# Optimization experiments

Measured on AMD Instinct MI355X. Metric: run time of the kernel, lower is better.

The kernel has to match this reference:

```python
import jax, jax.numpy as jnp
import numpy as np
from jax import lax

EPS = 1e-5  # BatchNorm eps (eval mode, running stats)
HEADS = 8

# --- surrogate-gradient Heaviside (sigmoid surrogate, alpha=4) ---
@jax.custom_vjp
def spike(u):
    return (u >= 0.0).astype(u.dtype)

def _spike_fwd(u):
    return spike(u), u

def _spike_bwd(u, g):
    s = jax.nn.sigmoid(4.0 * u)
    return (g * 4.0 * s * (1.0 - s),)

spike.defvjp(_spike_fwd, _spike_bwd)

def lif(x, tau=0.5, threshold=1.0):
    """Multi-step LIF over leading time axis: v_t = tau*v_{t-1} + x_t,
    s_t = H(v_t - threshold), hard reset v_t *= (1 - s_t)."""
    def step(v, xt):
        v = tau * v + xt
        s = spike(v - threshold)
        return v * (1.0 - s), s
    _, out = lax.scan(step, jnp.zeros_like(x[0]), x)
    return out

def bn_eval(x, gamma, beta, mean, var):
    # x: (T,B,C,N); per-channel affine using running stats
    inv = gamma / jnp.sqrt(var + EPS)
    return x * inv[None, None, :, None] + (beta - mean * inv)[None, None, :, None]

def setup_inputs() -> dict:
    key = jax.random.key(0)
    ks = jax.random.split(key, 12)
    T, B, C, H, W = 4, 32, 384, 16, 16
    d = {}
    d['x'] = jax.random.normal(ks[0], (T, B, C, H, W), dtype=jnp.float32)
    # 1x1 Conv1d weights == (C_out, C_in) matrices
    sc = 1.0 / np.sqrt(C)
    d['q_w'] = jax.random.normal(ks[1], (C, C), dtype=jnp.float32) * sc
    d['q_gamma'] = jnp.ones((C,), jnp.float32)
    d['q_beta'] = jnp.zeros((C,), jnp.float32)
    d['q_mean'] = jax.random.normal(ks[2], (C,), dtype=jnp.float32) * 0.1
    d['q_var'] = jax.random.uniform(ks[3], (C,), dtype=jnp.float32) + 0.5
    d['k_w'] = jax.random.normal(ks[4], (C, C), dtype=jnp.float32) * sc
    d['k_gamma'] = jnp.ones((C,), jnp.float32)
    d['k_beta'] = jnp.zeros((C,), jnp.float32)
    d['k_mean'] = jax.random.normal(ks[5], (C,), dtype=jnp.float32) * 0.1
    d['k_var'] = jax.random.uniform(ks[6], (C,), dtype=jnp.float32) + 0.5
    d['proj_w'] = jax.random.normal(ks[7], (C, C), dtype=jnp.float32) * sc
    d['proj_b'] = jax.random.normal(ks[8], (C,), dtype=jnp.float32) * 0.01
    d['proj_gamma'] = jnp.ones((C,), jnp.float32)
    d['proj_beta'] = jnp.zeros((C,), jnp.float32)
    d['proj_mean'] = jax.random.normal(ks[9], (C,), dtype=jnp.float32) * 0.1
    d['proj_var'] = jax.random.uniform(ks[10], (C,), dtype=jnp.float32) + 0.5
    d['mem_alpha'] = jnp.float32(0.2)
    return d

def reference(x, q_w, q_gamma, q_beta, q_mean, q_var,
              k_w, k_gamma, k_beta, k_mean, k_var,
              proj_w, proj_b, proj_gamma, proj_beta, proj_mean, proj_var,
              mem_alpha):
    T, B, C, H, W = x.shape
    Hh = HEADS
    Dh = C // Hh
    N = H * W
    # proj_lif applied to raw input, then flatten spatial dims
    s = lif(x, tau=0.5, threshold=1.0).reshape(T, B, C, N)
    # q path: 1x1 conv (channel GEMM) -> BN -> LIF
    q = lif(bn_eval(jnp.einsum('tbcn,dc->tbdn', s, q_w), q_gamma, q_beta, q_mean, q_var),
            tau=0.5, threshold=1.0).reshape(T, B, Hh, Dh, N)
    # k path
    k = lif(bn_eval(jnp.einsum('tbcn,dc->tbdn', s, k_w), k_gamma, k_beta, k_mean, k_var),
            tau=0.5, threshold=1.0).reshape(T, B, Hh, Dh, N)
    # temporal decayed memory: m_0 = q_0; m_t = alpha*m_{t-1} + (1-alpha)*q_{t-1}
    def mstep(m_prev, q_prev):
        m = mem_alpha * m_prev + (1.0 - mem_alpha) * q_prev
        return m, m
    _, mems_rest = lax.scan(mstep, q[0], q[:-1])
    mems = jnp.concatenate([q[:1], mems_rest], axis=0)  # (T,B,Hh,Dh,N)
    # cat along Dh then sum == sum(mems)+sum(q)
    q_sum = jnp.sum(mems, axis=3, keepdims=True) + jnp.sum(q, axis=3, keepdims=True)
    attn = lif(q_sum, tau=0.5, threshold=0.5)  # (T,B,Hh,1,N)
    y = (attn * k).reshape(T, B, C, N)
    # proj conv (with bias) -> BN -> reshape back to (T,B,C,H,W)
    y = jnp.einsum('tbcn,dc->tbdn', y, proj_w) + proj_b[None, None, :, None]
    y = bn_eval(y, proj_gamma, proj_beta, proj_mean, proj_var)
    return y.reshape(T, B, C, H, W)
```

## Files before the change

### kernel.cpp

```cpp
#include <hip/hip_runtime.h>

#define T_ 4
#define B_ 32
#define C_ 384
#define N_ 256
#define HEADS_ 8
#define DH_ 48
#define EPS_ 1e-5f
#define NW_ (C_*C_)

typedef _Float16 f16;
typedef __attribute__((ext_vector_type(8))) _Float16 f16x8;
typedef __attribute__((ext_vector_type(16))) float f32x16;

#define PSCALE     4096.0f
#define PSCALE_INV (1.0f/4096.0f)

__global__ __launch_bounds__(256)
void prep_kernel(const float* __restrict__ x, f16* __restrict__ s,
                 const float* __restrict__ qw, const float* __restrict__ kw,
                 const float* __restrict__ pw,
                 f16* __restrict__ q2, f16* __restrict__ k2, f16* __restrict__ p2)
{
    __shared__ f16 Ls[64][72];
    if (blockIdx.z == 32) {
        int idx = (blockIdx.y * 4 + blockIdx.x) * 256 + threadIdx.x;
#pragma unroll
        for (int it = 0; it < 24; ++it) {
            {
                float w = qw[idx]; f16 a = (f16)w; f16 bb = (f16)((w - (float)a) * PSCALE);
                q2[idx] = a; q2[NW_ + idx] = bb;
            }
            {
                float w = kw[idx]; f16 a = (f16)w; f16 bb = (f16)((w - (float)a) * PSCALE);
                k2[idx] = a; k2[NW_ + idx] = bb;
            }
            {
                float w = pw[idx]; f16 a = (f16)w; f16 bb = (f16)((w - (float)a) * PSCALE);
                p2[idx] = a; p2[NW_ + idx] = bb;
            }
            idx += 6144;
        }
        return;
    }

    const int tid = threadIdx.x;
    const int n0 = blockIdx.x * 64;
    const int c0 = blockIdx.y * 64;
    const int b  = blockIdx.z;
    const int cl = tid >> 4;
    const int nl = (tid & 15) * 4;

    float v[4][4];
#pragma unroll
    for (int i = 0; i < 4; ++i)
#pragma unroll
        for (int j = 0; j < 4; ++j) v[i][j] = 0.f;

    for (int t = 0; t < T_; ++t) {
        const float* xt = x + (((size_t)t * B_ + b) * C_) * N_;
#pragma unroll
        for (int i = 0; i < 4; ++i) {
            int c = c0 + cl + 16 * i;
            float4 xv = *(const float4*)&xt[(size_t)c * N_ + n0 + nl];
            float xa[4] = {xv.x, xv.y, xv.z, xv.w};
#pragma unroll
            for (int j = 0; j < 4; ++j) {
                float vv = 0.5f * v[i][j] + xa[j];
                int sp = (vv >= 1.0f) ? 1 : 0;
                v[i][j] = sp ? 0.f : vv;
                Ls[nl + j][cl + 16 * i] = sp ? (f16)1.0f : (f16)0.0f;
            }
        }
        __syncthreads();
        {
            int r = tid >> 2, ch = (tid & 3) * 16;
            uint4 w0 = *(const uint4*)&Ls[r][ch];
            uint4 w1 = *(const uint4*)&Ls[r][ch + 8];
            f16* dst = s + (((size_t)t * B_ + b) * N_ + n0 + r) * (size_t)C_ + c0 + ch;
            *(uint4*)dst = w0;
            *(uint4*)(dst + 8) = w1;
        }
        __syncthreads();
    }
}

__global__ __launch_bounds__(256)
void qk_gemm_lif_kernel(const f16* __restrict__ Wq, const f16* __restrict__ Wk,
                        const f16* __restrict__ S,
                        const float* __restrict__ qg, const float* __restrict__ qb,
                        const float* __restrict__ qm, const float* __restrict__ qv,
                        const float* __restrict__ kg, const float* __restrict__ kb,
                        const float* __restrict__ km, const float* __restrict__ kv,
                        f16* __restrict__ q_spk, f16* __restrict__ k_spk)
{
    __shared__ __align__(16) char smem[36864];
    f16 (*As)[72]      = reinterpret_cast<f16(*)[72]>(smem);
    f16 (*Bs)[64][72]  = reinterpret_cast<f16(*)[64][72]>(smem + 18432);
    float (*P)[64]     = reinterpret_cast<float(*)[64]>(smem);

    const int tid  = threadIdx.x;
    const int lane = tid & 63;
    const int wave = tid >> 6;
    const int wm = wave & 1, wd = wave >> 1;
    const int l31 = lane & 31;
    const int lhi = lane >> 5;

    const int mb = blockIdx.x;
    const int b  = mb >> 3;
    const int n0 = (mb & 7) * 32;
    const int dp0 = blockIdx.y * 64;
    const int path = (dp0 >= C_) ? 1 : 0;
    const int d0 = dp0 - path * C_;

    const f16* W = path ? Wk : Wq;
    const float* g_  = path ? kg : qg;
    const float* be_ = path ? kb : qb;
    const float* m_  = path ? km : qm;
    const float* va_ = path ? kv : qv;
    f16* spk = path ? k_spk : q_spk;

    const int dcol = d0 + wd * 32 + l31;
    const float inv = g_[dcol] / sqrtf(va_[dcol] + EPS_);
    const float add = be_[dcol] - m_[dcol] * inv;

    const int ar = tid >> 1;
    const int ah = (tid & 1) * 32;
    const int at = ar >> 5;
    const int an = n0 + (ar & 31);
    const f16* arow = S + (((size_t)at * B_ + b) * N_ + an) * (size_t)C_;

    const int bp = tid >> 7;
    const int brr = (tid >> 1) & 63;
    const int bh = (tid & 1) * 32;
    const f16* brow = W + (size_t)bp * NW_ + (size_t)(d0 + brr) * C_;

    f32x16 acc[2][2];
#pragma unroll
    for (int ms = 0; ms < 2; ++ms)
#pragma unroll
        for (int p = 0; p < 2; ++p)
#pragma unroll
            for (int r = 0; r < 16; ++r) acc[ms][p][r] = 0.f;

    for (int kc = 0; kc < C_; kc += 64) {
        __syncthreads();
        {
            const f16* ga = arow + kc + ah;
            *(uint4*)&As[ar][ah]      = *(const uint4*)(ga);
            *(uint4*)&As[ar][ah + 8]  = *(const uint4*)(ga + 8);
            *(uint4*)&As[ar][ah + 16] = *(const uint4*)(ga + 16);
            *(uint4*)&As[ar][ah + 24] = *(const uint4*)(ga + 24);
            const f16* gb = brow + kc + bh;
            *(uint4*)&Bs[bp][brr][bh]      = *(const uint4*)(gb);
            *(uint4*)&Bs[bp][brr][bh + 8]  = *(const uint4*)(gb + 8);
            *(uint4*)&Bs[bp][brr][bh + 16] = *(const uint4*)(gb + 16);
            *(uint4*)&Bs[bp][brr][bh + 24] = *(const uint4*)(gb + 24);
        }
        __syncthreads();
#pragma unroll
        for (int kk = 0; kk < 4; ++kk) {
            const int ko = kk * 16 + lhi * 8;
            f16x8 a0 = *(const f16x8*)&As[wm * 64 + l31][ko];
            f16x8 a1 = *(const f16x8*)&As[wm * 64 + 32 + l31][ko];
            f16x8 b0 = *(const f16x8*)&Bs[0][wd * 32 + l31][ko];
            f16x8 b1 = *(const f16x8*)&Bs[1][wd * 32 + l31][ko];
            acc[0][0] = __builtin_amdgcn_mfma_f32_32x32x16_f16(a0, b0, acc[0][0], 0, 0, 0);
            acc[1][0] = __builtin_amdgcn_mfma_f32_32x32x16_f16(a1, b0, acc[1][0], 0, 0, 0);
            acc[0][1] = __builtin_amdgcn_mfma_f32_32x32x16_f16(a0, b1, acc[0][1], 0, 0, 0);
            acc[1][1] = __builtin_amdgcn_mfma_f32_32x32x16_f16(a1, b1, acc[1][1], 0, 0, 0);
        }
    }

    __syncthreads();
#pragma unroll
    for (int ms = 0; ms < 2; ++ms)
#pragma unroll
    for (int r = 0; r < 16; ++r) {
        int row = wm * 64 + ms * 32 + (r & 3) + 8 * (r >> 2) + 4 * lhi;
        float val = acc[ms][0][r] + acc[ms][1][r] * PSCALE_INV;
        P[row][wd * 32 + l31] = val * inv + add;
    }
    __syncthreads();

    {
        const int d = tid & 63;
        const int g = tid >> 6;
#pragma unroll
        for (int i = 0; i < 8; ++i) {
            const int nl = g + 4 * i;
            float v = 0.f;
#pragma unroll
            for (int t = 0; t < T_; ++t) {
                float p = P[t * 32 + nl][d];
                float vv = 0.5f * v + p;
                int sp = (vv >= 1.0f) ? 1 : 0;
                v = sp ? 0.f : vv;
                spk[(((size_t)t * B_ + b) * N_ + n0 + nl) * C_ + d0 + d] =
                    sp ? (f16)1.0f : (f16)0.0f;
            }
        }
    }
}

__global__ __launch_bounds__(256)
void head_attn_kernel(const f16* __restrict__ q_spk,
                      const float* __restrict__ alpha_p,
                      unsigned char* __restrict__ attn)
{
    int i = blockIdx.x * 256 + threadIdx.x;
    int n = i & (N_ - 1);
    int h = (i >> 8) & (HEADS_ - 1);
    int b = i >> 11;
    const float alpha = alpha_p[0];
    const int stride = B_ * HEADS_ * N_;
    float M = 0.f, v = 0.f, Sprev = 0.f;
#pragma unroll
    for (int t = 0; t < T_; ++t) {
        const uint4* p = (const uint4*)(q_spk + (((size_t)(t * B_ + b) * N_) + n) * C_ + h * DH_);
        int cnt = 0;
#pragma unroll
        for (int j = 0; j < 6; ++j) {
            uint4 w = p[j];
            cnt += __popc(w.x & 0x04000400u) + __popc(w.y & 0x04000400u)
                 + __popc(w.z & 0x04000400u) + __popc(w.w & 0x04000400u);
        }
        float Sqt = (float)cnt;
        if (t == 0) M = Sqt;
        else        M = alpha * M + (1.f - alpha) * Sprev;
        float qsum = M + Sqt;
        float vv = 0.5f * v + qsum;
        unsigned char sp = (vv >= 0.5f) ? 1 : 0;
        v = sp ? 0.f : vv;
        attn[(size_t)t * stride + i] = sp;
        Sprev = Sqt;
    }
}

__global__ __launch_bounds__(256)
void proj_gemm_kernel(const f16* __restrict__ Wp,
                      const f16* __restrict__ K,
                      const unsigned char* __restrict__ attn,
                      const float* __restrict__ bias,
                      const float* __restrict__ gamma, const float* __restrict__ beta,
                      const float* __restrict__ mean,  const float* __restrict__ var,
                      float* __restrict__ out)
{
    __shared__ __align__(16) char smem[36864];
    f16 (*As)[72]     = reinterpret_cast<f16(*)[72]>(smem);
    f16 (*Bs)[64][72] = reinterpret_cast<f16(*)[64][72]>(smem + 18432);

    const int tid  = threadIdx.x;
    const int lane = tid & 63;
    const int wave = tid >> 6;
    const int wm = wave & 1, wd = wave >> 1;
    const int l31 = lane & 31;
    const int lhi = lane >> 5;

    const int mb = blockIdx.x;
    const int tb = mb >> 1;
    const int n0 = (mb & 1) * 128;
    const int d0 = blockIdx.y * 64;

    const int dcol = d0 + wd * 32 + l31;
    const float iv = gamma[dcol] / sqrtf(var[dcol] + EPS_);
    const float ad = beta[dcol] - mean[dcol] * iv + bias[dcol] * iv;

    const int ar = tid >> 1;
    const int ah = (tid & 1) * 32;
    const int an = n0 + ar;
    const f16* arow = K + ((size_t)tb * N_ + an) * (size_t)C_;
    const unsigned char* At = attn + (size_t)tb * HEADS_ * N_;

    const int bp = tid >> 7;
    const int brr = (tid >> 1) & 63;
    const int bh = (tid & 1) * 32;
    const f16* brow = Wp + (size_t)bp * NW_ + (size_t)(d0 + brr) * C_;

    f32x16 acc[2][2];
#pragma unroll
    for (int ms = 0; ms < 2; ++ms)
#pragma unroll
        for (int p = 0; p < 2; ++p)
#pragma unroll
            for (int r = 0; r < 16; ++r) acc[ms][p][r] = 0.f;

    for (int kc = 0; kc < C_; kc += 64) {
        __syncthreads();
        {
#pragma unroll
            for (int j = 0; j < 4; ++j) {
                int c = kc + ah + 8 * j;
                int h = c / DH_;
                unsigned char am = At[(size_t)h * N_ + an];
                uint4 val = am ? *(const uint4*)(arow + c) : make_uint4(0u, 0u, 0u, 0u);
                *(uint4*)&As[ar][ah + 8 * j] = val;
            }
            const f16* gb = brow + kc + bh;
            *(uint4*)&Bs[bp][brr][bh]      = *(const uint4*)(gb);
            *(uint4*)&Bs[bp][brr][bh + 8]  = *(const uint4*)(gb + 8);
            *(uint4*)&Bs[bp][brr][bh + 16] = *(const uint4*)(gb + 16);
            *(uint4*)&Bs[bp][brr][bh + 24] = *(const uint4*)(gb + 24);
        }
        __syncthreads();
#pragma unroll
        for (int kk = 0; kk < 4; ++kk) {
            const int ko = kk * 16 + lhi * 8;
            f16x8 a0 = *(const f16x8*)&As[wm * 64 + l31][ko];
            f16x8 a1 = *(const f16x8*)&As[wm * 64 + 32 + l31][ko];
            f16x8 b0 = *(const f16x8*)&Bs[0][wd * 32 + l31][ko];
            f16x8 b1 = *(const f16x8*)&Bs[1][wd * 32 + l31][ko];
            acc[0][0] = __builtin_amdgcn_mfma_f32_32x32x16_f16(a0, b0, acc[0][0], 0, 0, 0);
            acc[1][0] = __builtin_amdgcn_mfma_f32_32x32x16_f16(a1, b0, acc[1][0], 0, 0, 0);
            acc[0][1] = __builtin_amdgcn_mfma_f32_32x32x16_f16(a0, b1, acc[0][1], 0, 0, 0);
            acc[1][1] = __builtin_amdgcn_mfma_f32_32x32x16_f16(a1, b1, acc[1][1], 0, 0, 0);
        }
    }

    float* obase = out + ((size_t)tb * C_ + dcol) * N_;
#pragma unroll
    for (int ms = 0; ms < 2; ++ms)
#pragma unroll
    for (int r = 0; r < 16; ++r) {
        int n = n0 + wm * 64 + ms * 32 + (r & 3) + 8 * (r >> 2) + 4 * lhi;
        float val = acc[ms][0][r] + acc[ms][1][r] * PSCALE_INV;
        obase[n] = val * iv + ad;
    }
}

extern "C" void kernel_launch(void* const* d_in, const int* in_sizes, int n_in,
                              void* d_out, int out_size, void* d_ws, size_t ws_size,
                              hipStream_t stream)
{
    const float* x       = (const float*)d_in[0];
    const float* q_w     = (const float*)d_in[1];
    const float* q_gamma = (const float*)d_in[2];
    const float* q_beta  = (const float*)d_in[3];
    const float* q_mean  = (const float*)d_in[4];
    const float* q_var   = (const float*)d_in[5];
    const float* k_w     = (const float*)d_in[6];
    const float* k_gamma = (const float*)d_in[7];
    const float* k_beta  = (const float*)d_in[8];
    const float* k_mean  = (const float*)d_in[9];
    const float* k_var   = (const float*)d_in[10];
    const float* proj_w  = (const float*)d_in[11];
    const float* proj_b  = (const float*)d_in[12];
    const float* p_gamma = (const float*)d_in[13];
    const float* p_beta  = (const float*)d_in[14];
    const float* p_mean  = (const float*)d_in[15];
    const float* p_var   = (const float*)d_in[16];
    const float* m_alpha = (const float*)d_in[17];

    float* out = (float*)d_out;

    const size_t SPK_BYTES = (size_t)T_ * B_ * N_ * C_ * sizeof(f16);
    const size_t W2_BYTES  = (size_t)2 * NW_ * sizeof(f16);

    unsigned char* ws = (unsigned char*)d_ws;
    size_t off = 0;
    auto carve = [&](size_t bytes) {
        off = (off + 255) & ~(size_t)255;
        void* p = ws + off;
        off += bytes;
        return p;
    };
    f16* s_f16  = (f16*)carve(SPK_BYTES);
    f16* q_spk  = (f16*)carve(SPK_BYTES);
    f16* k_spk  = (f16*)carve(SPK_BYTES);
    f16* Wq2    = (f16*)carve(W2_BYTES);
    f16* Wk2    = (f16*)carve(W2_BYTES);
    f16* Wp2    = (f16*)carve(W2_BYTES);
    unsigned char* attn = (unsigned char*)carve((size_t)T_ * B_ * HEADS_ * N_);

    dim3 pgrid1(4, 6, 33);
    prep_kernel<<<pgrid1, 256, 0, stream>>>(x, s_f16, q_w, k_w, proj_w, Wq2, Wk2, Wp2);

    dim3 qkgrid(256, 12);
    qk_gemm_lif_kernel<<<qkgrid, 256, 0, stream>>>(Wq2, Wk2, s_f16,
                                                   q_gamma, q_beta, q_mean, q_var,
                                                   k_gamma, k_beta, k_mean, k_var,
                                                   q_spk, k_spk);

    head_attn_kernel<<<(B_ * HEADS_ * N_) / 256, 256, 0, stream>>>(q_spk, m_alpha, attn);

    dim3 pjgrid(256, 6);
    proj_gemm_kernel<<<pjgrid, 256, 0, stream>>>(Wp2, k_spk, attn, proj_b,
                                                 p_gamma, p_beta, p_mean, p_var, out);
}
```

Baseline: 230.7 us.

## Fuse head attention into GEMM epilogues via per-head spike-count atomics

Result: slower. 238.2 us (+3.3%).

```diff
diff --git a/kernel.cpp b/kernel.cpp
--- a/kernel.cpp
+++ b/kernel.cpp
@@ -20,13 +20,14 @@
 void prep_kernel(const float* __restrict__ x, f16* __restrict__ s,
                  const float* __restrict__ qw, const float* __restrict__ kw,
                  const float* __restrict__ pw,
-                 f16* __restrict__ q2, f16* __restrict__ k2, f16* __restrict__ p2)
+                 f16* __restrict__ q2, f16* __restrict__ k2, f16* __restrict__ p2,
+                 unsigned int* __restrict__ counts)
 {
-    __shared__ f16 Ls[64][72];
     if (blockIdx.z == 32) {
-        int idx = (blockIdx.y * 4 + blockIdx.x) * 256 + threadIdx.x;
-#pragma unroll
-        for (int it = 0; it < 24; ++it) {
+        const int base = (blockIdx.y * 4 + blockIdx.x) * 256 + threadIdx.x;
+        int idx = base;
+#pragma unroll 4
+        for (int it = 0; it < 48; ++it) {
             {
                 float w = qw[idx]; f16 a = (f16)w; f16 bb = (f16)((w - (float)a) * PSCALE);
                 q2[idx] = a; q2[NW_ + idx] = bb;
@@ -39,49 +40,49 @@
                 float w = pw[idx]; f16 a = (f16)w; f16 bb = (f16)((w - (float)a) * PSCALE);
                 p2[idx] = a; p2[NW_ + idx] = bb;
             }
-            idx += 6144;
-        }
+            idx += 3072;
+        }
+        const uint4 z = make_uint4(0u, 0u, 0u, 0u);
+        for (int i = base; i < (T_ * B_ * HEADS_ * N_) / 4; i += 3072)
+            ((uint4*)counts)[i] = z;
         return;
     }
 
     const int tid = threadIdx.x;
-    const int n0 = blockIdx.x * 64;
-    const int c0 = blockIdx.y * 64;
+    const int ng = tid & 15;
+    const int cg = tid >> 4;
+    const int n4 = blockIdx.x * 64 + ng * 4;
+    const int c0 = blockIdx.y * 128 + cg * 8;
     const int b  = blockIdx.z;
-    const int cl = tid >> 4;
-    const int nl = (tid & 15) * 4;
-
-    float v[4][4];
-#pragma unroll
-    for (int i = 0; i < 4; ++i)
+
+    float v[8][4];
+#pragma unroll
+    for (int i = 0; i < 8; ++i)
 #pragma unroll
         for (int j = 0; j < 4; ++j) v[i][j] = 0.f;
 
+#pragma unroll
     for (int t = 0; t < T_; ++t) {
         const float* xt = x + (((size_t)t * B_ + b) * C_) * N_;
-#pragma unroll
-        for (int i = 0; i < 4; ++i) {
-            int c = c0 + cl + 16 * i;
-            float4 xv = *(const float4*)&xt[(size_t)c * N_ + n0 + nl];
-            float xa[4] = {xv.x, xv.y, xv.z, xv.w};
-#pragma unroll
-            for (int j = 0; j < 4; ++j) {
-                float vv = 0.5f * v[i][j] + xa[j];
+        float4 xv[8];
+#pragma unroll
+        for (int i = 0; i < 8; ++i)
+            xv[i] = *(const float4*)&xt[(size_t)(c0 + i) * N_ + n4];
+#pragma unroll
+        for (int j = 0; j < 4; ++j) {
+            union { f16 h[8]; uint4 q; } u;
+#pragma unroll
+            for (int i = 0; i < 8; ++i) {
+                float xa = (j == 0) ? xv[i].x : (j == 1) ? xv[i].y
+                         : (j == 2) ? xv[i].z : xv[i].w;
+                float vv = 0.5f * v[i][j] + xa;
                 int sp = (vv >= 1.0f) ? 1 : 0;
                 v[i][j] = sp ? 0.f : vv;
-                Ls[nl + j][cl + 16 * i] = sp ? (f16)1.0f : (f16)0.0f;
-            }
-        }
-        __syncthreads();
-        {
-            int r = tid >> 2, ch = (tid & 3) * 16;
-            uint4 w0 = *(const uint4*)&Ls[r][ch];
-            uint4 w1 = *(const uint4*)&Ls[r][ch + 8];
-            f16* dst = s + (((size_t)t * B_ + b) * N_ + n0 + r) * (size_t)C_ + c0 + ch;
-            *(uint4*)dst = w0;
-            *(uint4*)(dst + 8) = w1;
-        }
-        __syncthreads();
+                u.h[i] = sp ? (f16)1.0f : (f16)0.0f;
+            }
+            f16* dst = s + (((size_t)t * B_ + b) * N_ + n4 + j) * (size_t)C_ + c0;
+            *(uint4*)dst = u.q;
+        }
     }
 }
 
@@ -92,7 +93,7 @@
                         const float* __restrict__ qm, const float* __restrict__ qv,
                         const float* __restrict__ kg, const float* __restrict__ kb,
                         const float* __restrict__ km, const float* __restrict__ kv,
-                        f16* __restrict__ q_spk, f16* __restrict__ k_spk)
+                        unsigned int* __restrict__ counts, f16* __restrict__ k_spk)
 {
     __shared__ __align__(16) char smem[36864];
     f16 (*As)[72]      = reinterpret_cast<f16(*)[72]>(smem);
@@ -118,7 +119,6 @@
     const float* be_ = path ? kb : qb;
     const float* m_  = path ? km : qm;
     const float* va_ = path ? kv : qv;
-    f16* spk = path ? k_spk : q_spk;
 
     const int dcol = d0 + wd * 32 + l31;
     const float inv = g_[dcol] / sqrtf(va_[dcol] + EPS_);
@@ -186,69 +186,63 @@
     {
         const int d = tid & 63;
         const int g = tid >> 6;
-#pragma unroll
-        for (int i = 0; i < 8; ++i) {
-            const int nl = g + 4 * i;
-            float v = 0.f;
-#pragma unroll
-            for (int t = 0; t < T_; ++t) {
-                float p = P[t * 32 + nl][d];
-                float vv = 0.5f * v + p;
-                int sp = (vv >= 1.0f) ? 1 : 0;
-                v = sp ? 0.f : vv;
-                spk[(((size_t)t * B_ + b) * N_ + n0 + nl) * C_ + d0 + d] =
-                    sp ? (f16)1.0f : (f16)0.0f;
-            }
-        }
-    }
-}
-
-__global__ __launch_bounds__(256)
-void head_attn_kernel(const f16* __restrict__ q_spk,
-                      const float* __restrict__ alpha_p,
-                      unsigned char* __restrict__ attn)
-{
-    int i = blockIdx.x * 256 + threadIdx.x;
-    int n = i & (N_ - 1);
-    int h = (i >> 8) & (HEADS_ - 1);
-    int b = i >> 11;
-    const float alpha = alpha_p[0];
-    const int stride = B_ * HEADS_ * N_;
-    float M = 0.f, v = 0.f, Sprev = 0.f;
-#pragma unroll
-    for (int t = 0; t < T_; ++t) {
-        const uint4* p = (const uint4*)(q_spk + (((size_t)(t * B_ + b) * N_) + n) * C_ + h * DH_);
-        int cnt = 0;
-#pragma unroll
-        for (int j = 0; j < 6; ++j) {
-            uint4 w = p[j];
-            cnt += __popc(w.x & 0x04000400u) + __popc(w.y & 0x04000400u)
-                 + __popc(w.z & 0x04000400u) + __popc(w.w & 0x04000400u);
-        }
-        float Sqt = (float)cnt;
-        if (t == 0) M = Sqt;
-        else        M = alpha * M + (1.f - alpha) * Sprev;
-        float qsum = M + Sqt;
-        float vv = 0.5f * v + qsum;
-        unsigned char sp = (vv >= 0.5f) ? 1 : 0;
-        v = sp ? 0.f : vv;
-        attn[(size_t)t * stride + i] = sp;
-        Sprev = Sqt;
+        if (path == 0) {
+            const int h0 = d0 / DH_;
+            const int ls = (h0 + 1) * DH_ - d0;
+            const unsigned long long lom = (1ull << ls) - 1ull;
+#pragma unroll
+            for (int i = 0; i < 8; ++i) {
+                const int nl = g + 4 * i;
+                float v = 0.f;
+#pragma unroll
+                for (int t = 0; t < T_; ++t) {
+                    float p = P[t * 32 + nl][d];
+                    float vv = 0.5f * v + p;
+                    int sp = (vv >= 1.0f) ? 1 : 0;
+                    v = sp ? 0.f : vv;
+                    unsigned long long m = __ballot(sp);
+                    if (lane == 0) {
+                        const int base = ((t * B_ + b) * HEADS_) * N_ + n0 + nl;
+                        atomicAdd(&counts[base + h0 * N_],
+                                  (unsigned int)__popcll(m & lom));
+                        atomicAdd(&counts[base + (h0 + 1) * N_],
+                                  (unsigned int)__popcll(m & ~lom));
+                    }
+                }
+            }
+        } else {
+#pragma unroll
+            for (int i = 0; i < 8; ++i) {
+                const int nl = g + 4 * i;
+                float v = 0.f;
+#pragma unroll
+                for (int t = 0; t < T_; ++t) {
+                    float p = P[t * 32 + nl][d];
+                    float vv = 0.5f * v + p;
+                    int sp = (vv >= 1.0f) ? 1 : 0;
+                    v = sp ? 0.f : vv;
+                    k_spk[(((size_t)t * B_ + b) * N_ + n0 + nl) * C_ + d0 + d] =
+                        sp ? (f16)1.0f : (f16)0.0f;
+                }
+            }
+        }
     }
 }
 
 __global__ __launch_bounds__(256)
 void proj_gemm_kernel(const f16* __restrict__ Wp,
                       const f16* __restrict__ K,
-                      const unsigned char* __restrict__ attn,
+                      const unsigned int* __restrict__ counts,
+                      const float* __restrict__ alpha_p,
                       const float* __restrict__ bias,
                       const float* __restrict__ gamma, const float* __restrict__ beta,
                       const float* __restrict__ mean,  const float* __restrict__ var,
                       float* __restrict__ out)
 {
-    __shared__ __align__(16) char smem[36864];
+    __shared__ __align__(16) char smem[37888];
     f16 (*As)[72]     = reinterpret_cast<f16(*)[72]>(smem);
     f16 (*Bs)[64][72] = reinterpret_cast<f16(*)[64][72]>(smem + 18432);
+    unsigned char* attn_l = (unsigned char*)(smem + 36864);
 
     const int tid  = threadIdx.x;
     const int lane = tid & 63;
@@ -262,6 +256,31 @@
     const int n0 = (mb & 1) * 128;
     const int d0 = blockIdx.y * 64;
 
+    {
+        const int t = tb >> 5;
+        const int b = tb & 31;
+        const float alpha = alpha_p[0];
+        for (int ch = tid; ch < HEADS_ * 128; ch += 256) {
+            const int h  = ch >> 7;
+            const int nl = ch & 127;
+            const unsigned int* cp =
+                counts + ((size_t)b * HEADS_ + h) * N_ + n0 + nl;
+            float M = 0.f, v = 0.f, Sprev = 0.f;
+            unsigned char sp = 0;
+            for (int tp = 0; tp <= t; ++tp) {
+                float Sqt = (float)cp[(size_t)tp * (B_ * HEADS_ * N_)];
+                if (tp == 0) M = Sqt;
+                else         M = alpha * M + (1.f - alpha) * Sprev;
+                float qsum = M + Sqt;
+                float vv = 0.5f * v + qsum;
+                sp = (vv >= 0.5f) ? 1 : 0;
+                v = sp ? 0.f : vv;
+                Sprev = Sqt;
+            }
+            attn_l[ch] = sp;
+        }
+    }
+
     const int dcol = d0 + wd * 32 + l31;
     const float iv = gamma[dcol] / sqrtf(var[dcol] + EPS_);
     const float ad = beta[dcol] - mean[dcol] * iv + bias[dcol] * iv;
@@ -270,7 +289,6 @@
     const int ah = (tid & 1) * 32;
     const int an = n0 + ar;
     const f16* arow = K + ((size_t)tb * N_ + an) * (size_t)C_;
-    const unsigned char* At = attn + (size_t)tb * HEADS_ * N_;
 
     const int bp = tid >> 7;
     const int brr = (tid >> 1) & 63;
@@ -292,7 +310,7 @@
             for (int j = 0; j < 4; ++j) {
                 int c = kc + ah + 8 * j;
                 int h = c / DH_;
-                unsigned char am = At[(size_t)h * N_ + an];
+                unsigned char am = attn_l[h * 128 + ar];
                 uint4 val = am ? *(const uint4*)(arow + c) : make_uint4(0u, 0u, 0u, 0u);
                 *(uint4*)&As[ar][ah + 8 * j] = val;
             }
@@ -355,6 +373,7 @@
 
     const size_t SPK_BYTES = (size_t)T_ * B_ * N_ * C_ * sizeof(f16);
     const size_t W2_BYTES  = (size_t)2 * NW_ * sizeof(f16);
+    const size_t TBHN      = (size_t)T_ * B_ * HEADS_ * N_;
 
     unsigned char* ws = (unsigned char*)d_ws;
     size_t off = 0;
@@ -365,25 +384,23 @@
         return p;
     };
     f16* s_f16  = (f16*)carve(SPK_BYTES);
-    f16* q_spk  = (f16*)carve(SPK_BYTES);
     f16* k_spk  = (f16*)carve(SPK_BYTES);
     f16* Wq2    = (f16*)carve(W2_BYTES);
     f16* Wk2    = (f16*)carve(W2_BYTES);
     f16* Wp2    = (f16*)carve(W2_BYTES);
-    unsigned char* attn = (unsigned char*)carve((size_t)T_ * B_ * HEADS_ * N_);
-
-    dim3 pgrid1(4, 6, 33);
-    prep_kernel<<<pgrid1, 256, 0, stream>>>(x, s_f16, q_w, k_w, proj_w, Wq2, Wk2, Wp2);
+    unsigned int* counts = (unsigned int*)carve(TBHN * 4);
+
+    dim3 pgrid1(4, 3, 33);
+    prep_kernel<<<pgrid1, 256, 0, stream>>>(x, s_f16, q_w, k_w, proj_w,
+                                            Wq2, Wk2, Wp2, counts);
 
     dim3 qkgrid(256, 12);
     qk_gemm_lif_kernel<<<qkgrid, 256, 0, stream>>>(Wq2, Wk2, s_f16,
                                                    q_gamma, q_beta, q_mean, q_var,
                                                    k_gamma, k_beta, k_mean, k_var,
-                                                   q_spk, k_spk);
-
-    head_attn_kernel<<<(B_ * HEADS_ * N_) / 256, 256, 0, stream>>>(q_spk, m_alpha, attn);
+                                                   counts, k_spk);
 
     dim3 pjgrid(256, 6);
-    proj_gemm_kernel<<<pjgrid, 256, 0, stream>>>(Wp2, k_spk, attn, proj_b,
+    proj_gemm_kernel<<<pjgrid, 256, 0, stream>>>(Wp2, k_spk, counts, m_alpha, proj_b,
                                                  p_gamma, p_beta, p_mean, p_var, out);
 }
```

## Remove LDS staging in prep and qk GEMM LIF epilogues via row remapping

Applied to the files above, without the earlier changes.

New measurement: 230.8 us. No clear change (+0.0%).

```diff
diff --git a/kernel.cpp b/kernel.cpp
--- a/kernel.cpp
+++ b/kernel.cpp
@@ -22,11 +22,11 @@
                  const float* __restrict__ pw,
                  f16* __restrict__ q2, f16* __restrict__ k2, f16* __restrict__ p2)
 {
-    __shared__ f16 Ls[64][72];
     if (blockIdx.z == 32) {
-        int idx = (blockIdx.y * 4 + blockIdx.x) * 256 + threadIdx.x;
-#pragma unroll
-        for (int it = 0; it < 24; ++it) {
+        const int base = (blockIdx.y * 4 + blockIdx.x) * 256 + threadIdx.x;
+        int idx = base;
+#pragma unroll 4
+        for (int it = 0; it < 48; ++it) {
             {
                 float w = qw[idx]; f16 a = (f16)w; f16 bb = (f16)((w - (float)a) * PSCALE);
                 q2[idx] = a; q2[NW_ + idx] = bb;
@@ -39,49 +39,46 @@
                 float w = pw[idx]; f16 a = (f16)w; f16 bb = (f16)((w - (float)a) * PSCALE);
                 p2[idx] = a; p2[NW_ + idx] = bb;
             }
-            idx += 6144;
+            idx += 3072;
         }
         return;
     }
 
     const int tid = threadIdx.x;
-    const int n0 = blockIdx.x * 64;
-    const int c0 = blockIdx.y * 64;
+    const int ng = tid & 15;
+    const int cg = tid >> 4;
+    const int n4 = blockIdx.x * 64 + ng * 4;
+    const int c0 = blockIdx.y * 128 + cg * 8;
     const int b  = blockIdx.z;
-    const int cl = tid >> 4;
-    const int nl = (tid & 15) * 4;
-
-    float v[4][4];
-#pragma unroll
-    for (int i = 0; i < 4; ++i)
+
+    float v[8][4];
+#pragma unroll
+    for (int i = 0; i < 8; ++i)
 #pragma unroll
         for (int j = 0; j < 4; ++j) v[i][j] = 0.f;
 
+#pragma unroll
     for (int t = 0; t < T_; ++t) {
         const float* xt = x + (((size_t)t * B_ + b) * C_) * N_;
-#pragma unroll
-        for (int i = 0; i < 4; ++i) {
-            int c = c0 + cl + 16 * i;
-            float4 xv = *(const float4*)&xt[(size_t)c * N_ + n0 + nl];
-            float xa[4] = {xv.x, xv.y, xv.z, xv.w};
-#pragma unroll
-            for (int j = 0; j < 4; ++j) {
-                float vv = 0.5f * v[i][j] + xa[j];
+        float4 xv[8];
+#pragma unroll
+        for (int i = 0; i < 8; ++i)
+            xv[i] = *(const float4*)&xt[(size_t)(c0 + i) * N_ + n4];
+#pragma unroll
+        for (int j = 0; j < 4; ++j) {
+            union { f16 h[8]; uint4 q; } u;
+#pragma unroll
+            for (int i = 0; i < 8; ++i) {
+                float xa = (j == 0) ? xv[i].x : (j == 1) ? xv[i].y
+                         : (j == 2) ? xv[i].z : xv[i].w;
+                float vv = 0.5f * v[i][j] + xa;
                 int sp = (vv >= 1.0f) ? 1 : 0;
                 v[i][j] = sp ? 0.f : vv;
-                Ls[nl + j][cl + 16 * i] = sp ? (f16)1.0f : (f16)0.0f;
-            }
-        }
-        __syncthreads();
-        {
-            int r = tid >> 2, ch = (tid & 3) * 16;
-            uint4 w0 = *(const uint4*)&Ls[r][ch];
-            uint4 w1 = *(const uint4*)&Ls[r][ch + 8];
-            f16* dst = s + (((size_t)t * B_ + b) * N_ + n0 + r) * (size_t)C_ + c0 + ch;
-            *(uint4*)dst = w0;
-            *(uint4*)(dst + 8) = w1;
-        }
-        __syncthreads();
+                u.h[i] = sp ? (f16)1.0f : (f16)0.0f;
+            }
+            f16* dst = s + (((size_t)t * B_ + b) * N_ + n4 + j) * (size_t)C_ + c0;
+            *(uint4*)dst = u.q;
+        }
     }
 }
 
@@ -97,7 +94,6 @@
     __shared__ __align__(16) char smem[36864];
     f16 (*As)[72]      = reinterpret_cast<f16(*)[72]>(smem);
     f16 (*Bs)[64][72]  = reinterpret_cast<f16(*)[64][72]>(smem + 18432);
-    float (*P)[64]     = reinterpret_cast<float(*)[64]>(smem);
 
     const int tid  = threadIdx.x;
     const int lane = tid & 63;
@@ -106,12 +102,11 @@
     const int l31 = lane & 31;
     const int lhi = lane >> 5;
 
-    const int mb = blockIdx.x;
+    const int path = blockIdx.x & 1;
+    const int mb = blockIdx.x >> 1;
     const int b  = mb >> 3;
     const int n0 = (mb & 7) * 32;
-    const int dp0 = blockIdx.y * 64;
-    const int path = (dp0 >= C_) ? 1 : 0;
-    const int d0 = dp0 - path * C_;
+    const int d0 = blockIdx.y * 64;
 
     const f16* W = path ? Wk : Wq;
     const float* g_  = path ? kg : qg;
@@ -126,9 +121,7 @@
 
     const int ar = tid >> 1;
     const int ah = (tid & 1) * 32;
-    const int at = ar >> 5;
-    const int an = n0 + (ar & 31);
-    const f16* arow = S + (((size_t)at * B_ + b) * N_ + an) * (size_t)C_;
+    const f16* arow = S + (((size_t)(ar & 3) * B_ + b) * N_ + n0 + (ar >> 2)) * (size_t)C_;
 
     const int bp = tid >> 7;
     const int brr = (tid >> 1) & 63;
@@ -172,33 +165,21 @@
         }
     }
 
-    __syncthreads();
 #pragma unroll
     for (int ms = 0; ms < 2; ++ms)
 #pragma unroll
-    for (int r = 0; r < 16; ++r) {
-        int row = wm * 64 + ms * 32 + (r & 3) + 8 * (r >> 2) + 4 * lhi;
-        float val = acc[ms][0][r] + acc[ms][1][r] * PSCALE_INV;
-        P[row][wd * 32 + l31] = val * inv + add;
-    }
-    __syncthreads();
-
-    {
-        const int d = tid & 63;
-        const int g = tid >> 6;
-#pragma unroll
-        for (int i = 0; i < 8; ++i) {
-            const int nl = g + 4 * i;
-            float v = 0.f;
-#pragma unroll
-            for (int t = 0; t < T_; ++t) {
-                float p = P[t * 32 + nl][d];
-                float vv = 0.5f * v + p;
-                int sp = (vv >= 1.0f) ? 1 : 0;
-                v = sp ? 0.f : vv;
-                spk[(((size_t)t * B_ + b) * N_ + n0 + nl) * C_ + d0 + d] =
-                    sp ? (f16)1.0f : (f16)0.0f;
-            }
+    for (int g = 0; g < 4; ++g) {
+        const int n = n0 + wm * 16 + ms * 8 + 2 * g + lhi;
+        float v = 0.f;
+#pragma unroll
+        for (int t = 0; t < 4; ++t) {
+            const int r = g * 4 + t;
+            float val = (acc[ms][0][r] + acc[ms][1][r] * PSCALE_INV) * inv + add;
+            float vv = 0.5f * v + val;
+            int sp = (vv >= 1.0f) ? 1 : 0;
+            v = sp ? 0.f : vv;
+            spk[(((size_t)t * B_ + b) * N_ + n) * C_ + dcol] =
+                sp ? (f16)1.0f : (f16)0.0f;
         }
     }
 }
@@ -355,6 +336,7 @@
 
     const size_t SPK_BYTES = (size_t)T_ * B_ * N_ * C_ * sizeof(f16);
     const size_t W2_BYTES  = (size_t)2 * NW_ * sizeof(f16);
+    const size_t TBHN      = (size_t)T_ * B_ * HEADS_ * N_;
 
     unsigned char* ws = (unsigned char*)d_ws;
     size_t off = 0;
@@ -370,12 +352,13 @@
     f16* Wq2    = (f16*)carve(W2_BYTES);
     f16* Wk2    = (f16*)carve(W2_BYTES);
     f16* Wp2    = (f16*)carve(W2_BYTES);
-    unsigned char* attn = (unsigned char*)carve((size_t)T_ * B_ * HEADS_ * N_);
-
-    dim3 pgrid1(4, 6, 33);
-    prep_kernel<<<pgrid1, 256, 0, stream>>>(x, s_f16, q_w, k_w, proj_w, Wq2, Wk2, Wp2);
-
-    dim3 qkgrid(256, 12);
+    unsigned char* attn = (unsigned char*)carve(TBHN);
+
+    dim3 pgrid1(4, 3, 33);
+    prep_kernel<<<pgrid1, 256, 0, stream>>>(x, s_f16, q_w, k_w, proj_w,
+                                            Wq2, Wk2, Wp2);
+
+    dim3 qkgrid(512, 6);
     qk_gemm_lif_kernel<<<qkgrid, 256, 0, stream>>>(Wq2, Wk2, s_f16,
                                                    q_gamma, q_beta, q_mean, q_var,
                                                    k_gamma, k_beta, k_mean, k_var,
```
